# Optimization experiments

Measured on AMD Instinct MI355X. Metric: run time of the kernel, lower is better.

Reference implementation:

```python
import jax, jax.numpy as jnp
import numpy as np

NUM_SEGMENTS = 4096
N_NODES = 524288
D = 256


def setup_inputs() -> dict:
    key = jax.random.key(0)
    k1, k2, k3 = jax.random.split(key, 3)
    x = jax.random.normal(k1, (N_NODES, D), dtype=jnp.float32)
    batch = jnp.sort(jax.random.randint(k2, (N_NODES,), 0, NUM_SEGMENTS)).astype(jnp.int64)
    W = jax.random.normal(k3, (D, 1), dtype=jnp.float32) / np.sqrt(D)
    b = jnp.zeros((1,), dtype=jnp.float32)
    return {"x": x, "batch": batch, "W": W, "b": b}


def reference(x, batch, W, b):
    # gate_nn: Linear(in_features, 1) -> per-node scalar gate
    gate = (x @ W + b)[:, 0]                                  # [N]
    # segment-wise softmax over nodes sharing the same graph id
    seg_max = jax.ops.segment_max(gate, batch, num_segments=NUM_SEGMENTS)
    e = jnp.exp(gate - seg_max[batch])                        # [N]
    denom = jax.ops.segment_sum(e, batch, num_segments=NUM_SEGMENTS)
    alpha = e / denom[batch]                                  # [N]
    # attention-weighted sum pooling per graph
    out = jax.ops.segment_sum(x * alpha[:, None], batch, num_segments=NUM_SEGMENTS)
    return out  # [NUM_SEGMENTS, D]
```

## Files before the change

### kernel.cpp

```cpp
#include <hip/hip_runtime.h>


typedef float f32x4 __attribute__((ext_vector_type(4)));

__global__ void seg_bounds_kernel(const int* __restrict__ batch,
                                  int* __restrict__ seg_start,
                                  int n_nodes, int n_seg)
{
    const int i = blockIdx.x * blockDim.x + threadIdx.x;
    if (i >= n_nodes) return;
    const int cur  = batch[i];
    const int prev = (i == 0) ? -1 : batch[i - 1];
    for (int s = prev + 1; s <= cur; ++s) seg_start[s] = i;
    if (i == n_nodes - 1) {
        for (int s = cur + 1; s <= n_seg; ++s) seg_start[s] = n_nodes;
    }
}

__global__ __launch_bounds__(256, 6)
void gap_fused(const float* __restrict__ x,
               const int* __restrict__ seg_start,
               const float* __restrict__ W,
               float* __restrict__ out)
{
    const int seg   = blockIdx.x;
    const int start = seg_start[seg];
    const int end   = seg_start[seg + 1];

    const int tid  = threadIdx.x;
    const int lane = tid & 63;
    const int wave = tid >> 6;
    constexpr int NW = 4;
    constexpr int U  = 4;
    constexpr int STRIDE = NW * U;

    const f32x4 wv = reinterpret_cast<const f32x4*>(W)[lane];
    const f32x4* __restrict__ xv = reinterpret_cast<const f32x4*>(x);

    f32x4 acc = {0.f, 0.f, 0.f, 0.f};
    float den = 0.f;

    int base = start + wave * U;

    if (base < end) {
        const int last = end - 1;

        int r1 = (base + 1 < end) ? base + 1 : last;
        int r2 = (base + 2 < end) ? base + 2 : last;
        int r3 = (base + 3 < end) ? base + 3 : last;
        f32x4 c0 = __builtin_nontemporal_load(&xv[(size_t)base * 64 + lane]);
        f32x4 c1 = __builtin_nontemporal_load(&xv[(size_t)r1   * 64 + lane]);
        f32x4 c2 = __builtin_nontemporal_load(&xv[(size_t)r2   * 64 + lane]);
        f32x4 c3 = __builtin_nontemporal_load(&xv[(size_t)r3   * 64 + lane]);

        while (true) {
            const int next = base + STRIDE;
            const bool havenext = next < end;

            f32x4 p0, p1, p2, p3;
            if (havenext) {
                const int q1 = (next + 1 < end) ? next + 1 : last;
                const int q2 = (next + 2 < end) ? next + 2 : last;
                const int q3 = (next + 3 < end) ? next + 3 : last;
                p0 = __builtin_nontemporal_load(&xv[(size_t)next * 64 + lane]);
                p1 = __builtin_nontemporal_load(&xv[(size_t)q1   * 64 + lane]);
                p2 = __builtin_nontemporal_load(&xv[(size_t)q2   * 64 + lane]);
                p3 = __builtin_nontemporal_load(&xv[(size_t)q3   * 64 + lane]);
            }

            float d0 = c0.x * wv.x + c0.y * wv.y + c0.z * wv.z + c0.w * wv.w;
            float d1 = c1.x * wv.x + c1.y * wv.y + c1.z * wv.z + c1.w * wv.w;
            float d2 = c2.x * wv.x + c2.y * wv.y + c2.z * wv.z + c2.w * wv.w;
            float d3 = c3.x * wv.x + c3.y * wv.y + c3.z * wv.z + c3.w * wv.w;

#pragma unroll
            for (int off = 32; off >= 1; off >>= 1) {
                d0 += __shfl_xor(d0, off, 64);
                d1 += __shfl_xor(d1, off, 64);
                d2 += __shfl_xor(d2, off, 64);
                d3 += __shfl_xor(d3, off, 64);
            }

            const float e0 = __expf(d0);
            const float e1 = (base + 1 < end) ? __expf(d1) : 0.f;
            const float e2 = (base + 2 < end) ? __expf(d2) : 0.f;
            const float e3 = (base + 3 < end) ? __expf(d3) : 0.f;

            den   += (e0 + e1) + (e2 + e3);
            acc.x += e0 * c0.x + e1 * c1.x + e2 * c2.x + e3 * c3.x;
            acc.y += e0 * c0.y + e1 * c1.y + e2 * c2.y + e3 * c3.y;
            acc.z += e0 * c0.z + e1 * c1.z + e2 * c2.z + e3 * c3.z;
            acc.w += e0 * c0.w + e1 * c1.w + e2 * c2.w + e3 * c3.w;

            if (!havenext) break;
            c0 = p0; c1 = p1; c2 = p2; c3 = p3;
            base = next;
        }
    }

    __shared__ float acc_lds[NW][256];
    __shared__ float den_lds[NW];
    *reinterpret_cast<f32x4*>(&acc_lds[wave][lane * 4]) = acc;
    if (lane == 0) den_lds[wave] = den;
    __syncthreads();

    float total = (acc_lds[0][tid] + acc_lds[1][tid]) + (acc_lds[2][tid] + acc_lds[3][tid]);
    const float dtot = (den_lds[0] + den_lds[1]) + (den_lds[2] + den_lds[3]);
    const float r = (end > start) ? (total / dtot) : 0.f;
    __builtin_nontemporal_store(r, &out[(size_t)seg * 256 + tid]);
}

extern "C" void kernel_launch(void* const* d_in, const int* in_sizes, int n_in,
                              void* d_out, int out_size, void* d_ws, size_t ws_size,
                              hipStream_t stream) {
    const float* x     = (const float*)d_in[0];
    const int*   batch = (const int*)d_in[1];
    const float* W     = (const float*)d_in[2];
    float* out = (float*)d_out;

    const int n_nodes = in_sizes[1];
    const int n_seg   = out_size / 256;

    int* seg_start = (int*)d_ws;

    const int bs = 256;
    seg_bounds_kernel<<<(n_nodes + bs - 1) / bs, bs, 0, stream>>>(batch, seg_start, n_nodes, n_seg);
    gap_fused<<<n_seg, bs, 0, stream>>>(x, seg_start, W, out);
}
```

Baseline: 95.33 us.

## Split nodes into fixed chunks with LDS and global atomic segment accumulation

```diff
diff --git a/kernel.cpp b/kernel.cpp
--- a/kernel.cpp
+++ b/kernel.cpp
@@ -3,69 +3,101 @@
 
 typedef float f32x4 __attribute__((ext_vector_type(4)));
 
-__global__ void seg_bounds_kernel(const int* __restrict__ batch,
-                                  int* __restrict__ seg_start,
-                                  int n_nodes, int n_seg)
-{
-    const int i = blockIdx.x * blockDim.x + threadIdx.x;
-    if (i >= n_nodes) return;
-    const int cur  = batch[i];
-    const int prev = (i == 0) ? -1 : batch[i - 1];
-    for (int s = prev + 1; s <= cur; ++s) seg_start[s] = i;
-    if (i == n_nodes - 1) {
-        for (int s = cur + 1; s <= n_seg; ++s) seg_start[s] = n_nodes;
-    }
-}
+#define NSLOT 8
 
 __global__ __launch_bounds__(256, 6)
-void gap_fused(const float* __restrict__ x,
-               const int* __restrict__ seg_start,
+void gap_chunk(const float* __restrict__ x,
+               const int* __restrict__ batch,
                const float* __restrict__ W,
-               float* __restrict__ out)
-{
-    const int seg   = blockIdx.x;
-    const int start = seg_start[seg];
-    const int end   = seg_start[seg + 1];
-
+               float* __restrict__ num,
+               float* __restrict__ den,
+               int n_nodes, int n_blocks)
+{
     const int tid  = threadIdx.x;
     const int lane = tid & 63;
     const int wave = tid >> 6;
-    constexpr int NW = 4;
-    constexpr int U  = 4;
-    constexpr int STRIDE = NW * U;
+
+    const long long bb = blockIdx.x;
+    const int blo = (int)((bb * n_nodes) / n_blocks);
+    const int bhi = (int)(((bb + 1) * n_nodes) / n_blocks);
+    const int cnt = bhi - blo;
+
+    const int wlo = blo + (int)(((long long)cnt * wave) >> 2);
+    const int whi = blo + (int)(((long long)cnt * (wave + 1)) >> 2);
+
+    __shared__ float lds_num[NSLOT][256];
+    __shared__ float lds_den[NSLOT];
+    for (int i = tid; i < NSLOT * 256; i += 256) (&lds_num[0][0])[i] = 0.f;
+    if (tid < NSLOT) lds_den[tid] = 0.f;
+    __syncthreads();
+
+    const int seg0 = batch[blo];
 
     const f32x4 wv = reinterpret_cast<const f32x4*>(W)[lane];
     const f32x4* __restrict__ xv = reinterpret_cast<const f32x4*>(x);
 
     f32x4 acc = {0.f, 0.f, 0.f, 0.f};
-    float den = 0.f;
-
-    int base = start + wave * U;
-
-    if (base < end) {
-        const int last = end - 1;
-
-        int r1 = (base + 1 < end) ? base + 1 : last;
-        int r2 = (base + 2 < end) ? base + 2 : last;
-        int r3 = (base + 3 < end) ? base + 3 : last;
-        f32x4 c0 = __builtin_nontemporal_load(&xv[(size_t)base * 64 + lane]);
-        f32x4 c1 = __builtin_nontemporal_load(&xv[(size_t)r1   * 64 + lane]);
-        f32x4 c2 = __builtin_nontemporal_load(&xv[(size_t)r2   * 64 + lane]);
-        f32x4 c3 = __builtin_nontemporal_load(&xv[(size_t)r3   * 64 + lane]);
+    float dsum = 0.f;
+    int cur = -1;
+
+    auto flush = [&]() {
+        const int slot = cur - seg0;
+        if (slot >= 0 && slot < NSLOT) {
+            atomicAdd(&lds_num[slot][lane * 4 + 0], acc.x);
+            atomicAdd(&lds_num[slot][lane * 4 + 1], acc.y);
+            atomicAdd(&lds_num[slot][lane * 4 + 2], acc.z);
+            atomicAdd(&lds_num[slot][lane * 4 + 3], acc.w);
+            if (lane == 0) atomicAdd(&lds_den[slot], dsum);
+        } else {
+            atomicAdd(&num[(size_t)cur * 256 + lane * 4 + 0], acc.x);
+            atomicAdd(&num[(size_t)cur * 256 + lane * 4 + 1], acc.y);
+            atomicAdd(&num[(size_t)cur * 256 + lane * 4 + 2], acc.z);
+            atomicAdd(&num[(size_t)cur * 256 + lane * 4 + 3], acc.w);
+            if (lane == 0) atomicAdd(&den[cur], dsum);
+        }
+        acc.x = 0.f; acc.y = 0.f; acc.z = 0.f; acc.w = 0.f;
+        dsum = 0.f;
+    };
+
+    int base = wlo;
+    if (base < whi) {
+        const int last = whi - 1;
+        cur = batch[base];
+
+        int s0, s1, s2, s3;
+        f32x4 c0, c1, c2, c3;
+        {
+            const int r1 = (base + 1 <= last) ? base + 1 : last;
+            const int r2 = (base + 2 <= last) ? base + 2 : last;
+            const int r3 = (base + 3 <= last) ? base + 3 : last;
+            c0 = __builtin_nontemporal_load(&xv[(size_t)base * 64 + lane]);
+            c1 = __builtin_nontemporal_load(&xv[(size_t)r1   * 64 + lane]);
+            c2 = __builtin_nontemporal_load(&xv[(size_t)r2   * 64 + lane]);
+            c3 = __builtin_nontemporal_load(&xv[(size_t)r3   * 64 + lane]);
+            s0 = batch[base];
+            s1 = (base + 1 <= last) ? batch[base + 1] : -1;
+            s2 = (base + 2 <= last) ? batch[base + 2] : -1;
+            s3 = (base + 3 <= last) ? batch[base + 3] : -1;
+        }
 
         while (true) {
-            const int next = base + STRIDE;
-            const bool havenext = next < end;
+            const int next = base + 4;
+            const bool havenext = next <= last;
 
             f32x4 p0, p1, p2, p3;
+            int t0 = -1, t1 = -1, t2 = -1, t3 = -1;
             if (havenext) {
-                const int q1 = (next + 1 < end) ? next + 1 : last;
-                const int q2 = (next + 2 < end) ? next + 2 : last;
-                const int q3 = (next + 3 < end) ? next + 3 : last;
+                const int q1 = (next + 1 <= last) ? next + 1 : last;
+                const int q2 = (next + 2 <= last) ? next + 2 : last;
+                const int q3 = (next + 3 <= last) ? next + 3 : last;
                 p0 = __builtin_nontemporal_load(&xv[(size_t)next * 64 + lane]);
                 p1 = __builtin_nontemporal_load(&xv[(size_t)q1   * 64 + lane]);
                 p2 = __builtin_nontemporal_load(&xv[(size_t)q2   * 64 + lane]);
                 p3 = __builtin_nontemporal_load(&xv[(size_t)q3   * 64 + lane]);
+                t0 = batch[next];
+                t1 = (next + 1 <= last) ? batch[next + 1] : -1;
+                t2 = (next + 2 <= last) ? batch[next + 2] : -1;
+                t3 = (next + 3 <= last) ? batch[next + 3] : -1;
             }
 
             float d0 = c0.x * wv.x + c0.y * wv.y + c0.z * wv.z + c0.w * wv.w;
@@ -81,33 +113,127 @@
                 d3 += __shfl_xor(d3, off, 64);
             }
 
-            const float e0 = __expf(d0);
-            const float e1 = (base + 1 < end) ? __expf(d1) : 0.f;
-            const float e2 = (base + 2 < end) ? __expf(d2) : 0.f;
-            const float e3 = (base + 3 < end) ? __expf(d3) : 0.f;
-
-            den   += (e0 + e1) + (e2 + e3);
-            acc.x += e0 * c0.x + e1 * c1.x + e2 * c2.x + e3 * c3.x;
-            acc.y += e0 * c0.y + e1 * c1.y + e2 * c2.y + e3 * c3.y;
-            acc.z += e0 * c0.z + e1 * c1.z + e2 * c2.z + e3 * c3.z;
-            acc.w += e0 * c0.w + e1 * c1.w + e2 * c2.w + e3 * c3.w;
+            const float e0 = (s0 >= 0) ? __expf(d0) : 0.f;
+            const float e1 = (s1 >= 0) ? __expf(d1) : 0.f;
+            const float e2 = (s2 >= 0) ? __expf(d2) : 0.f;
+            const float e3 = (s3 >= 0) ? __expf(d3) : 0.f;
+
+            if (s0 == cur && (s1 == cur || s1 < 0) &&
+                (s2 == cur || s2 < 0) && (s3 == cur || s3 < 0)) {
+                dsum  += (e0 + e1) + (e2 + e3);
+                acc.x += e0 * c0.x + e1 * c1.x + e2 * c2.x + e3 * c3.x;
+                acc.y += e0 * c0.y + e1 * c1.y + e2 * c2.y + e3 * c3.y;
+                acc.z += e0 * c0.z + e1 * c1.z + e2 * c2.z + e3 * c3.z;
+                acc.w += e0 * c0.w + e1 * c1.w + e2 * c2.w + e3 * c3.w;
+            } else {
+                if (s0 >= 0) {
+                    if (s0 != cur) { flush(); cur = s0; }
+                    dsum += e0;
+                    acc.x += e0 * c0.x; acc.y += e0 * c0.y;
+                    acc.z += e0 * c0.z; acc.w += e0 * c0.w;
+                }
+                if (s1 >= 0) {
+                    if (s1 != cur) { flush(); cur = s1; }
+                    dsum += e1;
+                    acc.x += e1 * c1.x; acc.y += e1 * c1.y;
+                    acc.z += e1 * c1.z; acc.w += e1 * c1.w;
+                }
+                if (s2 >= 0) {
+                    if (s2 != cur) { flush(); cur = s2; }
+                    dsum += e2;
+                    acc.x += e2 * c2.x; acc.y += e2 * c2.y;
+                    acc.z += e2 * c2.z; acc.w += e2 * c2.w;
+                }
+                if (s3 >= 0) {
+                    if (s3 != cur) { flush(); cur = s3; }
+                    dsum += e3;
+                    acc.x += e3 * c3.x; acc.y += e3 * c3.y;
+                    acc.z += e3 * c3.z; acc.w += e3 * c3.w;
+                }
+            }
 
             if (!havenext) break;
             c0 = p0; c1 = p1; c2 = p2; c3 = p3;
+            s0 = t0; s1 = t1; s2 = t2; s3 = t3;
             base = next;
         }
-    }
-
-    __shared__ float acc_lds[NW][256];
-    __shared__ float den_lds[NW];
+        flush();
+    }
+    __syncthreads();
+
+    const int seg_last = batch[bhi - 1];
+    int nslots = seg_last - seg0 + 1;
+    if (nslots > NSLOT) nslots = NSLOT;
+    for (int s = 0; s < nslots; ++s) {
+        const float v = lds_num[s][tid];
+        if (v != 0.f) atomicAdd(&num[(size_t)(seg0 + s) * 256 + tid], v);
+        if (tid == 0) {
+            const float dv = lds_den[s];
+            if (dv != 0.f) atomicAdd(&den[seg0 + s], dv);
+        }
+    }
+}
+
+__global__ void gap_combine(const float* __restrict__ num,
+                            const float* __restrict__ den,
+                            float* __restrict__ out, int n_seg)
+{
+    const int seg = blockIdx.x;
+    const int t   = threadIdx.x;
+    const float d = den[seg];
+    const float v = num[(size_t)seg * 256 + t];
+    const float r = (d > 0.f) ? v / d : 0.f;
+    __builtin_nontemporal_store(r, &out[(size_t)seg * 256 + t]);
+}
+
+__global__ void seg_bounds_kernel(const int* __restrict__ batch,
+                                  int* __restrict__ seg_start,
+                                  int n_nodes, int n_seg)
+{
+    const int i = blockIdx.x * blockDim.x + threadIdx.x;
+    if (i >= n_nodes) return;
+    const int curv = batch[i];
+    const int prev = (i == 0) ? -1 : batch[i - 1];
+    for (int s = prev + 1; s <= curv; ++s) seg_start[s] = i;
+    if (i == n_nodes - 1)
+        for (int s = curv + 1; s <= n_seg; ++s) seg_start[s] = n_nodes;
+}
+
+__global__ __launch_bounds__(256, 6)
+void gap_fused(const float* __restrict__ x,
+               const int* __restrict__ seg_start,
+               const float* __restrict__ W,
+               float* __restrict__ out)
+{
+    const int seg   = blockIdx.x;
+    const int start = seg_start[seg];
+    const int end   = seg_start[seg + 1];
+    const int tid  = threadIdx.x;
+    const int lane = tid & 63;
+    const int wave = tid >> 6;
+
+    const f32x4 wv = reinterpret_cast<const f32x4*>(W)[lane];
+    const f32x4* __restrict__ xv = reinterpret_cast<const f32x4*>(x);
+    f32x4 acc = {0.f, 0.f, 0.f, 0.f};
+    float den = 0.f;
+
+    for (int row = start + wave; row < end; row += 4) {
+        const f32x4 v = xv[(size_t)row * 64 + lane];
+        float d = v.x * wv.x + v.y * wv.y + v.z * wv.z + v.w * wv.w;
+#pragma unroll
+        for (int off = 32; off >= 1; off >>= 1) d += __shfl_xor(d, off, 64);
+        const float e = __expf(d);
+        den += e;
+        acc.x += e * v.x; acc.y += e * v.y; acc.z += e * v.z; acc.w += e * v.w;
+    }
+    __shared__ float acc_lds[4][256];
+    __shared__ float den_lds[4];
     *reinterpret_cast<f32x4*>(&acc_lds[wave][lane * 4]) = acc;
     if (lane == 0) den_lds[wave] = den;
     __syncthreads();
-
     float total = (acc_lds[0][tid] + acc_lds[1][tid]) + (acc_lds[2][tid] + acc_lds[3][tid]);
     const float dtot = (den_lds[0] + den_lds[1]) + (den_lds[2] + den_lds[3]);
-    const float r = (end > start) ? (total / dtot) : 0.f;
-    __builtin_nontemporal_store(r, &out[(size_t)seg * 256 + tid]);
+    out[(size_t)seg * 256 + tid] = (end > start) ? (total / dtot) : 0.f;
 }
 
 extern "C" void kernel_launch(void* const* d_in, const int* in_sizes, int n_in,
@@ -121,9 +247,17 @@
     const int n_nodes = in_sizes[1];
     const int n_seg   = out_size / 256;
 
-    int* seg_start = (int*)d_ws;
-
-    const int bs = 256;
-    seg_bounds_kernel<<<(n_nodes + bs - 1) / bs, bs, 0, stream>>>(batch, seg_start, n_nodes, n_seg);
-    gap_fused<<<n_seg, bs, 0, stream>>>(x, seg_start, W, out);
-}
+    const size_t need = (size_t)n_seg * 256 * sizeof(float) + (size_t)n_seg * sizeof(float);
+    if (ws_size >= need) {
+        float* num = (float*)d_ws;
+        float* den = num + (size_t)n_seg * 256;
+        hipMemsetAsync(d_ws, 0, need, stream);
+        const int G = 1536;
+        gap_chunk<<<G, 256, 0, stream>>>(x, batch, W, num, den, n_nodes, G);
+        gap_combine<<<n_seg, 256, 0, stream>>>(num, den, out, n_seg);
+    } else {
+        int* seg_start = (int*)d_ws;
+        seg_bounds_kernel<<<(n_nodes + 255) / 256, 256, 0, stream>>>(batch, seg_start, n_nodes, n_seg);
+        gap_fused<<<n_seg, 256, 0, stream>>>(x, seg_start, W, out);
+    }
+}
```

After: 144.9 us. 52.0% more time.

## Process each segment with a single wave instead of a four-wave block

Applied to the files above, without the earlier changes.

```diff
diff --git a/kernel.cpp b/kernel.cpp
--- a/kernel.cpp
+++ b/kernel.cpp
@@ -17,22 +17,16 @@
     }
 }
 
-__global__ __launch_bounds__(256, 6)
-void gap_fused(const float* __restrict__ x,
-               const int* __restrict__ seg_start,
-               const float* __restrict__ W,
-               float* __restrict__ out)
+__global__ __launch_bounds__(64, 4)
+void gap_wave(const float* __restrict__ x,
+              const int* __restrict__ seg_start,
+              const float* __restrict__ W,
+              float* __restrict__ out)
 {
     const int seg   = blockIdx.x;
     const int start = seg_start[seg];
     const int end   = seg_start[seg + 1];
-
-    const int tid  = threadIdx.x;
-    const int lane = tid & 63;
-    const int wave = tid >> 6;
-    constexpr int NW = 4;
-    constexpr int U  = 4;
-    constexpr int STRIDE = NW * U;
+    const int lane  = threadIdx.x;
 
     const f32x4 wv = reinterpret_cast<const f32x4*>(W)[lane];
     const f32x4* __restrict__ xv = reinterpret_cast<const f32x4*>(x);
@@ -40,28 +34,27 @@
     f32x4 acc = {0.f, 0.f, 0.f, 0.f};
     float den = 0.f;
 
-    int base = start + wave * U;
-
+    int base = start;
     if (base < end) {
         const int last = end - 1;
 
-        int r1 = (base + 1 < end) ? base + 1 : last;
-        int r2 = (base + 2 < end) ? base + 2 : last;
-        int r3 = (base + 3 < end) ? base + 3 : last;
+        int r1 = (base + 1 <= last) ? base + 1 : last;
+        int r2 = (base + 2 <= last) ? base + 2 : last;
+        int r3 = (base + 3 <= last) ? base + 3 : last;
         f32x4 c0 = __builtin_nontemporal_load(&xv[(size_t)base * 64 + lane]);
         f32x4 c1 = __builtin_nontemporal_load(&xv[(size_t)r1   * 64 + lane]);
         f32x4 c2 = __builtin_nontemporal_load(&xv[(size_t)r2   * 64 + lane]);
         f32x4 c3 = __builtin_nontemporal_load(&xv[(size_t)r3   * 64 + lane]);
 
         while (true) {
-            const int next = base + STRIDE;
-            const bool havenext = next < end;
+            const int next = base + 4;
+            const bool havenext = next <= last;
 
             f32x4 p0, p1, p2, p3;
             if (havenext) {
-                const int q1 = (next + 1 < end) ? next + 1 : last;
-                const int q2 = (next + 2 < end) ? next + 2 : last;
-                const int q3 = (next + 3 < end) ? next + 3 : last;
+                const int q1 = (next + 1 <= last) ? next + 1 : last;
+                const int q2 = (next + 2 <= last) ? next + 2 : last;
+                const int q3 = (next + 3 <= last) ? next + 3 : last;
                 p0 = __builtin_nontemporal_load(&xv[(size_t)next * 64 + lane]);
                 p1 = __builtin_nontemporal_load(&xv[(size_t)q1   * 64 + lane]);
                 p2 = __builtin_nontemporal_load(&xv[(size_t)q2   * 64 + lane]);
@@ -82,9 +75,9 @@
             }
 
             const float e0 = __expf(d0);
-            const float e1 = (base + 1 < end) ? __expf(d1) : 0.f;
-            const float e2 = (base + 2 < end) ? __expf(d2) : 0.f;
-            const float e3 = (base + 3 < end) ? __expf(d3) : 0.f;
+            const float e1 = (base + 1 <= last) ? __expf(d1) : 0.f;
+            const float e2 = (base + 2 <= last) ? __expf(d2) : 0.f;
+            const float e3 = (base + 3 <= last) ? __expf(d3) : 0.f;
 
             den   += (e0 + e1) + (e2 + e3);
             acc.x += e0 * c0.x + e1 * c1.x + e2 * c2.x + e3 * c3.x;
@@ -98,16 +91,14 @@
         }
     }
 
-    __shared__ float acc_lds[NW][256];
-    __shared__ float den_lds[NW];
-    *reinterpret_cast<f32x4*>(&acc_lds[wave][lane * 4]) = acc;
-    if (lane == 0) den_lds[wave] = den;
-    __syncthreads();
-
-    float total = (acc_lds[0][tid] + acc_lds[1][tid]) + (acc_lds[2][tid] + acc_lds[3][tid]);
-    const float dtot = (den_lds[0] + den_lds[1]) + (den_lds[2] + den_lds[3]);
-    const float r = (end > start) ? (total / dtot) : 0.f;
-    __builtin_nontemporal_store(r, &out[(size_t)seg * 256 + tid]);
+    f32x4 r;
+    if (end > start) {
+        const float inv = 1.0f / den;
+        r.x = acc.x * inv; r.y = acc.y * inv; r.z = acc.z * inv; r.w = acc.w * inv;
+    } else {
+        r.x = 0.f; r.y = 0.f; r.z = 0.f; r.w = 0.f;
+    }
+    __builtin_nontemporal_store(r, &reinterpret_cast<f32x4*>(out)[(size_t)seg * 64 + lane]);
 }
 
 extern "C" void kernel_launch(void* const* d_in, const int* in_sizes, int n_in,
@@ -123,7 +114,6 @@
 
     int* seg_start = (int*)d_ws;
 
-    const int bs = 256;
-    seg_bounds_kernel<<<(n_nodes + bs - 1) / bs, bs, 0, stream>>>(batch, seg_start, n_nodes, n_seg);
-    gap_fused<<<n_seg, bs, 0, stream>>>(x, seg_start, W, out);
+    seg_bounds_kernel<<<(n_nodes + 255) / 256, 256, 0, stream>>>(batch, seg_start, n_nodes, n_seg);
+    gap_wave<<<n_seg, 64, 0, stream>>>(x, seg_start, W, out);
 }
```

Result: no change. 96.45 us (+1.2%).
